# Optimization experiments

Measured on AMD Instinct MI355X. Metric: run time of the kernel, lower is better.

The kernel has to match this reference:

```python
import jax, jax.numpy as jnp
import numpy as np

N_NODES = 100000
N_EDGES = 1600000
F_IN = 35
F_OUT = 5
K = 3
HID = 100


def setup_inputs() -> dict:
    key = jax.random.key(0)
    ks = jax.random.split(key, 20)
    p = lambda k, shape: (jax.random.normal(k, shape, dtype=jnp.float32) * 0.1)
    inp = {
        "x": jax.random.normal(ks[0], (N_NODES, F_IN), dtype=jnp.float32),
        "edge_index": jax.random.randint(ks[1], (2, N_EDGES), 0, N_NODES, dtype=jnp.int64),
        "edge_weight": jax.random.uniform(ks[2], (N_EDGES,), dtype=jnp.float32),
        # MLP warm-start: Linear(35,100) -> ReLU -> Linear(100,5)
        "W1": p(ks[3], (F_IN, HID)), "b1": p(ks[4], (HID,)),
        "W2": p(ks[5], (HID, F_OUT)), "b2": p(ks[6], (F_OUT,)),
        # DCRNN gates: DConv weights [2 directions, K, in+out, out]
        "Wz": p(ks[7], (2, K, F_IN + F_OUT, F_OUT)), "bz": p(ks[8], (F_OUT,)),
        "Wr": p(ks[9], (2, K, F_IN + F_OUT, F_OUT)), "br": p(ks[10], (F_OUT,)),
        "Wh": p(ks[11], (2, K, F_IN + F_OUT, F_OUT)), "bh": p(ks[12], (F_OUT,)),
        # head Linear(5,1)
        "Wl": p(ks[13], (F_OUT, 1)), "bl": p(ks[14], (1,)),
    }
    return inp


def reference(x, edge_index, edge_weight, W1, b1, W2, b2, Wz, bz, Wr, br, Wh, bh, Wl, bl):
    n = x.shape[0]
    src, dst = edge_index[0], edge_index[1]
    eps = jnp.asarray(1e-12, x.dtype)
    # random-walk normalization: forward (out-degree) and backward (in-degree) diffusion
    deg_out = jax.ops.segment_sum(edge_weight, src, num_segments=n)
    deg_in = jax.ops.segment_sum(edge_weight, dst, num_segments=n)
    w_fwd = edge_weight / jnp.maximum(deg_out[src], eps)  # [E]
    w_bwd = edge_weight / jnp.maximum(deg_in[dst], eps)   # [E]

    def prop_fwd(X):  # aggregate src -> dst
        return jax.ops.segment_sum(X[src] * w_fwd[:, None], dst, num_segments=n)

    def prop_bwd(X):  # aggregate dst -> src (reversed edges)
        return jax.ops.segment_sum(X[dst] * w_bwd[:, None], src, num_segments=n)

    def dconv(X, W, b):  # W: [2, K, Cin, Cout]
        k_steps = W.shape[1]
        out = X @ W[0, 0] + X @ W[1, 0]
        if k_steps > 1:
            Tf0, Tb0 = X, X
            Tf1, Tb1 = prop_fwd(X), prop_bwd(X)
            out = out + Tf1 @ W[0, 1] + Tb1 @ W[1, 1]
            for k in range(2, k_steps):
                Tf2 = 2.0 * prop_fwd(Tf1) - Tf0
                Tb2 = 2.0 * prop_bwd(Tb1) - Tb0
                out = out + Tf2 @ W[0, k] + Tb2 @ W[1, k]
                Tf0, Tf1 = Tf1, Tf2
                Tb0, Tb1 = Tb1, Tb2
        return out + b

    # MLP warm-start hidden state
    h1 = jax.nn.relu(x @ W1 + b1) @ W2 + b2  # [N, F_OUT]

    # DCRNN GRU cell
    XH = jnp.concatenate([x, h1], axis=1)           # [N, F_IN+F_OUT]
    Z = jax.nn.sigmoid(dconv(XH, Wz, bz))
    R = jax.nn.sigmoid(dconv(XH, Wr, br))
    XHr = jnp.concatenate([x, h1 * R], axis=1)
    H_tilde = jnp.tanh(dconv(XHr, Wh, bh))
    H = Z * h1 + (1.0 - Z) * H_tilde                # [N, F_OUT]

    y = jax.nn.relu(H) @ Wl + bl                    # [N, 1]
    A = w_fwd                                        # normalized adjacency weights [E]
    return y, A
```

## Files before the change

kernel.cpp:

```cpp
#include <hip/hip_runtime.h>
#include <hip/hip_fp16.h>

#define F_IN 35
#define F_OUT 5
#define HID 100
#define BSH 8
#define BMSK 255
#define MAXB 512
#define NBLK 128

__device__ __forceinline__ unsigned qenc(float w) {
  unsigned b = __float_as_uint(w);
  int e = 127 - (int)((b >> 23) & 0xFF);
  unsigned m = (b >> 12) & 0x7FFu;
  if (e < 0) { e = 0; m = 0; }
  if (e > 15) { e = 15; m = 0; }
  return ((unsigned)e << 11) | m;
}
__device__ __forceinline__ float qdec(unsigned q) {
  return __uint_as_float(((127u - (q >> 11)) << 23) | ((q & 0x7FFu) << 12));
}

__device__ __forceinline__ float2 uph2(unsigned u) {
  __half2 h = *reinterpret_cast<const __half2*>(&u);
  return __half22float2(h);
}
__device__ __forceinline__ unsigned pkh2(float a, float b) {
  __half2 h = __floats2half2_rn(a, b);
  return *reinterpret_cast<const unsigned*>(&h);
}

__device__ __forceinline__ int ntli(const int* p) {
  return __builtin_nontemporal_load(p);
}
__device__ __forceinline__ float ntlf(const float* p) {
  return __builtin_nontemporal_load(p);
}
__device__ __forceinline__ long long ntll(const long long* p) {
  return __builtin_nontemporal_load(p);
}
__device__ __forceinline__ void ntsf(float* p, float v) {
  __builtin_nontemporal_store(v, p);
}

__global__ __launch_bounds__(256) void prep_weights(
    const float* __restrict__ Wz, const float* __restrict__ Wr,
    const float* __restrict__ Wh, const float* __restrict__ W1,
    float* __restrict__ W1t, float* __restrict__ WpackAt,
    float* __restrict__ WpackCxt, float* __restrict__ WpackCh) {
  int t = blockIdx.x * blockDim.x + threadIdx.x;
  auto W = [&](const float* Wp, int d, int k, int i, int o) {
    return Wp[((d * 3 + k) * 40 + i) * 5 + o];
  };
  auto wa = [&](int i, int c) -> float {
    if (c < 5)  return W(Wz,0,0,i,c)+W(Wz,1,0,i,c)-W(Wz,0,2,i,c)-W(Wz,1,2,i,c);
    if (c < 10) return W(Wr,0,0,i,c-5)+W(Wr,1,0,i,c-5)-W(Wr,0,2,i,c-5)-W(Wr,1,2,i,c-5);
    if (c < 15) return W(Wz,0,1,i,c-10);
    if (c < 20) return W(Wr,0,1,i,c-15);
    if (c < 25) return W(Wz,0,2,i,c-20);
    if (c < 30) return W(Wr,0,2,i,c-25);
    if (c < 35) return W(Wz,1,1,i,c-30);
    if (c < 40) return W(Wr,1,1,i,c-35);
    if (c < 45) return W(Wz,1,2,i,c-40);
    return W(Wr,1,2,i,c-45);
  };
  auto wc = [&](int i, int c) -> float {
    if (c < 5)  return W(Wh,0,0,i,c)+W(Wh,1,0,i,c)-W(Wh,0,2,i,c)-W(Wh,1,2,i,c);
    if (c < 10) return W(Wh,0,1,i,c-5);
    if (c < 15) return W(Wh,0,2,i,c-10);
    if (c < 20) return W(Wh,1,1,i,c-15);
    return W(Wh,1,2,i,c-20);
  };
  if (t < 3500) {
    int hh = t / 35, i = t % 35;
    W1t[t] = W1[i * HID + hh];
  } else if (t < 5500) {
    int u = t - 3500; int c = u / 40, i = u % 40;
    WpackAt[u] = wa(i, c);
  } else if (t < 6375) {
    int u = t - 5500; int c = u / 35, i = u % 35;
    WpackCxt[u] = wc(i, c);
  } else if (t < 6500) {
    int u = t - 6375; int o = u / 25, c = u % 25;
    WpackCh[u] = wc(F_IN + o, c);
  }
}

__global__ __launch_bounds__(1024) void passB_kernel(
    const int* __restrict__ ei, const float* __restrict__ w,
    int2* __restrict__ staged_f, int2* __restrict__ staged_b,
    int* __restrict__ lomat, int E) {
  __shared__ int hh[MAXB], sc[MAXB], cc[MAXB];
  int dir = blockIdx.y;
  int j = blockIdx.x;
  int tid = threadIdx.x;
  for (int k = tid; k < MAXB; k += blockDim.x) { hh[k] = 0; cc[k] = 0; }
  __syncthreads();
  size_t c0 = (size_t)j * E / NBLK;
  size_t c1 = (size_t)(j + 1) * E / NBLK;
  const int* keyc = dir ? ei : ei + E;
  const int* othc = dir ? ei + E : ei;
  int2* staged = dir ? staged_b : staged_f;
  int* lom = lomat + ((size_t)dir * NBLK + j) * (MAXB + 1);
  for (size_t e = c0 + tid; e < c1; e += blockDim.x) {
    int key = ntli(keyc + e);
    atomicAdd(&hh[key >> BSH], 1);
  }
  __syncthreads();
  if (tid < MAXB) sc[tid] = hh[tid];
  __syncthreads();
  for (int off = 1; off < MAXB; off <<= 1) {
    int a = (tid >= off && tid < MAXB) ? sc[tid - off] : 0;
    __syncthreads();
    if (tid < MAXB) sc[tid] += a;
    __syncthreads();
  }
  if (tid < MAXB) {
    int lo = sc[tid] - hh[tid];
    lom[tid] = lo;
    hh[tid] = lo;
  }
  if (tid == 0) lom[MAXB] = (int)(c1 - c0);
  __syncthreads();
  for (size_t e = c0 + tid; e < c1; e += blockDim.x) {
    int key = ntli(keyc + e);
    int oth = ntli(othc + e);
    unsigned q = qenc(ntlf(w + e));
    int b = key >> BSH;
    int p = hh[b] + atomicAdd(&cc[b], 1);
    staged[c0 + p] = make_int2(oth | ((key & BMSK) << 17), (int)q);
  }
}

__global__ __launch_bounds__(512) void scanb2_kernel(
    const int* __restrict__ lomat,
    int* __restrict__ bbase_f, int* __restrict__ bbase_b,
    int* __restrict__ rs_f, int* __restrict__ rs_b,
    int nbuck, int N, int E) {
  __shared__ int s0[MAXB], s1[MAXB];
  int t = threadIdx.x;
  int cf = 0, cb = 0;
  if (t < nbuck) {
    for (int j = 0; j < NBLK; j++) {
      const int* lf = lomat + (size_t)j * (MAXB + 1);
      const int* lb = lomat + ((size_t)NBLK + j) * (MAXB + 1);
      cf += lf[t + 1] - lf[t];
      cb += lb[t + 1] - lb[t];
    }
  }
  s0[t] = cf; s1[t] = cb;
  __syncthreads();
  for (int off = 1; off < MAXB; off <<= 1) {
    int a = (t >= off) ? s0[t - off] : 0;
    int b = (t >= off) ? s1[t - off] : 0;
    __syncthreads();
    s0[t] += a; s1[t] += b;
    __syncthreads();
  }
  bbase_f[t + 1] = s0[t];
  bbase_b[t + 1] = s1[t];
  if (t == 0) { bbase_f[0] = 0; bbase_b[0] = 0; rs_f[N] = E; rs_b[N] = E; }
}

__global__ __launch_bounds__(256) void passC_kernel(
    const int2* __restrict__ staged_f, const int2* __restrict__ staged_b,
    const int* __restrict__ lomat,
    const int* __restrict__ bbase_f, const int* __restrict__ bbase_b,
    int* __restrict__ adj_f, int* __restrict__ adj_b,
    int* __restrict__ rs_f, int* __restrict__ rs_b,
    float* __restrict__ inv_in, float* __restrict__ inv_out, int N, int E) {
  int dir = blockIdx.y;
  const long long* staged =
      (const long long*)(dir ? staged_b : staged_f);
  const int* lomd = lomat + (size_t)dir * NBLK * (MAXB + 1);
  const int* bbase = dir ? bbase_b : bbase_f;
  int* adj = dir ? adj_b : adj_f;
  int* rs  = dir ? rs_b : rs_f;
  float* inv = dir ? inv_out : inv_in;
  int b = blockIdx.x;
  int base = bbase[b];
  __shared__ int cnt[256]; __shared__ float wsum[256];
  __shared__ int loc[256]; __shared__ int cur[256];
  int tid = threadIdx.x;
  int wave = tid >> 6, lane = tid & 63;
  cnt[tid] = 0; wsum[tid] = 0.f; cur[tid] = 0;
  __syncthreads();
  int j0 = wave * 32;
  int lo0k = 0, lo1k = 0;
  if (lane < 32) {
    const int* lj = lomd + (size_t)(j0 + lane) * (MAXB + 1);
    lo0k = lj[b];
    lo1k = lj[b + 1];
  }
  for (int k = 0; k < 32; k++) {
    int lo0 = __shfl(lo0k, k);
    int lo1 = __shfl(lo1k, k);
    if (lo0 >= lo1) continue;
    size_t cj = (size_t)(j0 + k) * E / NBLK;
    for (int i = lo0 + lane; i < lo1; i += 64) {
      long long it = ntll(staged + cj + i);
      int idv = (int)(unsigned)(it & 0xFFFFFFFFll);
      unsigned q = (unsigned)((unsigned long long)it >> 32);
      int nl = (idv >> 17) & BMSK;
      atomicAdd(&cnt[nl], 1);
      atomicAdd(&wsum[nl], qdec(q));
    }
  }
  __syncthreads();
  int v = cnt[tid];
  loc[tid] = v;
  __syncthreads();
  for (int off = 1; off < 256; off <<= 1) {
    int a = (tid >= off) ? loc[tid - off] : 0;
    __syncthreads();
    loc[tid] += a;
    __syncthreads();
  }
  int excl = loc[tid] - v;
  int node = (b << BSH) + tid;
  if (node < N) {
    rs[node] = base + excl;
    inv[node] = 1.f / fmaxf(wsum[tid], 1e-12f);
  }
  __syncthreads();
  loc[tid] = excl;
  __syncthreads();
  for (int k = 0; k < 32; k++) {
    int lo0 = __shfl(lo0k, k);
    int lo1 = __shfl(lo1k, k);
    if (lo0 >= lo1) continue;
    size_t cj = (size_t)(j0 + k) * E / NBLK;
    for (int i = lo0 + lane; i < lo1; i += 64) {
      long long it = ntll(staged + cj + i);
      int idv = (int)(unsigned)(it & 0xFFFFFFFFll);
      int q = (int)((unsigned long long)it >> 32);
      int nl = (idv >> 17) & BMSK;
      int p = base + loc[nl] + atomicAdd(&cur[nl], 1);
      adj[p] = (idv & 0x1FFFF) | (q << 17);
    }
  }
}

__global__ __launch_bounds__(256) void wfout_kernel(
    const int* __restrict__ ei, const float* __restrict__ ew,
    const float* __restrict__ inv_out, float* __restrict__ wf, int E) {
  for (int e = blockIdx.x * blockDim.x + threadIdx.x; e < E;
       e += gridDim.x * blockDim.x)
    ntsf(wf + e, ntlf(ew + e) * inv_out[ntli(ei + e)]);
}

__global__ __launch_bounds__(256) void nodeA_kernel(
    const float* __restrict__ x,
    const float* __restrict__ W1t, const float* __restrict__ b1,
    const float* __restrict__ W2, const float* __restrict__ b2,
    const float* __restrict__ bz, const float* __restrict__ br,
    const float* __restrict__ WpackAt, const float* __restrict__ WpackCxt,
    const float* __restrict__ inv_out, const float* __restrict__ inv_in,
    float* __restrict__ h1, float* __restrict__ accDz,
    float* __restrict__ accDr, __half* __restrict__ PA_f,
    __half* __restrict__ PA_b, __half* __restrict__ accCx, int N) {
  __shared__ float part[4][64][5];
  int tid = threadIdx.x;
  int lane = tid & 63;
  int q = __builtin_amdgcn_readfirstlane(tid >> 6);
  int n = blockIdx.x * 64 + lane;
  bool act = n < N;
  float xv[40];
  const float* xr = x + (size_t)n * F_IN;
  #pragma unroll
  for (int i = 0; i < F_IN; i++) xv[i] = act ? xr[i] : 0.f;

  float h5[5] = {0.f, 0.f, 0.f, 0.f, 0.f};
  int hbase = q * 25;
  for (int k = 0; k < 25; k++) {
    int hh = hbase + k;
    const float* w1r = W1t + hh * F_IN;
    float a = b1[hh];
    #pragma unroll
    for (int i = 0; i < F_IN; i++) a = fmaf(xv[i], w1r[i], a);
    a = fmaxf(a, 0.f);
    #pragma unroll
    for (int o = 0; o < 5; o++) h5[o] = fmaf(a, W2[hh * 5 + o], h5[o]);
  }
  #pragma unroll
  for (int o = 0; o < 5; o++) part[q][lane][o] = h5[o];
  __syncthreads();
  #pragma unroll
  for (int o = 0; o < 5; o++) {
    h5[o] = part[0][lane][o] + part[1][lane][o] + part[2][lane][o] +
            part[3][lane][o] + b2[o];
    xv[F_IN + o] = h5[o];
  }
  if (!act) return;
  if (q == 0) {
    #pragma unroll
    for (int o = 0; o < 5; o++) h1[(size_t)n * 5 + o] = h5[o];
  }
  float sOut = inv_out[n], sIn = inv_in[n];
  int c0 = q * 19, c1 = min(c0 + 19, 75);
  for (int c = c0; c < c1; c++) {
    float a = 0.f;
    if (c < 50) {
      const float* wr = WpackAt + c * 40;
      #pragma unroll
      for (int i = 0; i < 40; i++) a = fmaf(xv[i], wr[i], a);
    } else {
      const float* wr = WpackCxt + (c - 50) * F_IN;
      #pragma unroll
      for (int i = 0; i < F_IN; i++) a = fmaf(xv[i], wr[i], a);
    }
    if (c < 5)       accDz[(size_t)n * 5 + c] = a + bz[c];
    else if (c < 10) accDr[(size_t)n * 5 + (c - 5)] = a + br[c - 5];
    else if (c < 30) PA_f[(size_t)n * 20 + (c - 10)] = __float2half(a * sOut);
    else if (c < 50) PA_b[(size_t)n * 20 + (c - 30)] = __float2half(a * sIn);
    else             accCx[(size_t)n * 25 + (c - 50)] = __float2half(a);
  }
}

__global__ __launch_bounds__(256) void p1_kernel(
    const int* __restrict__ rs_f, const int* __restrict__ rs_b,
    const int* __restrict__ adj_f, const int* __restrict__ adj_b,
    const __half* __restrict__ PA_f, const __half* __restrict__ PA_b,
    const float* __restrict__ inv_out, const float* __restrict__ inv_in,
    float* __restrict__ Q1_f, float* __restrict__ Q1_b,
    __half* __restrict__ Q2_f, __half* __restrict__ Q2_b, int N) {
  int dir = blockIdx.x & 1;
  int idx = (blockIdx.x >> 1) * 256 + threadIdx.x;
  if (idx >= 2 * N) return;
  int n = idx >> 1, half = idx & 1;
  const int* rs  = dir ? rs_b : rs_f;
  const int* adj = dir ? adj_b : adj_f;
  const __half* PA = dir ? PA_b : PA_f;
  int i0 = rs[n], i1 = rs[n + 1];
  float acc[10];
  #pragma unroll
  for (int c = 0; c < 10; c++) acc[c] = 0.f;
  int i = i0;
  for (; i + 4 <= i1; i += 4) {
    int a0 = ntli(adj + i),     a1 = ntli(adj + i + 1),
        a2 = ntli(adj + i + 2), a3 = ntli(adj + i + 3);
    const unsigned* r0 = (const unsigned*)(PA + (size_t)(a0 & 0x1FFFF) * 20) + half * 5;
    const unsigned* r1 = (const unsigned*)(PA + (size_t)(a1 & 0x1FFFF) * 20) + half * 5;
    const unsigned* r2 = (const unsigned*)(PA + (size_t)(a2 & 0x1FFFF) * 20) + half * 5;
    const unsigned* r3 = (const unsigned*)(PA + (size_t)(a3 & 0x1FFFF) * 20) + half * 5;
    unsigned u0[5], u1[5], u2[5], u3[5];
    #pragma unroll
    for (int k = 0; k < 5; k++) u0[k] = r0[k];
    #pragma unroll
    for (int k = 0; k < 5; k++) u1[k] = r1[k];
    #pragma unroll
    for (int k = 0; k < 5; k++) u2[k] = r2[k];
    #pragma unroll
    for (int k = 0; k < 5; k++) u3[k] = r3[k];
    float w0 = qdec(((unsigned)a0) >> 17), w1 = qdec(((unsigned)a1) >> 17),
          w2 = qdec(((unsigned)a2) >> 17), w3 = qdec(((unsigned)a3) >> 17);
    #pragma unroll
    for (int k = 0; k < 5; k++) {
      float2 f0 = uph2(u0[k]), f1 = uph2(u1[k]), f2 = uph2(u2[k]), f3 = uph2(u3[k]);
      acc[2*k]   = fmaf(w0, f0.x, acc[2*k]);   acc[2*k+1] = fmaf(w0, f0.y, acc[2*k+1]);
      acc[2*k]   = fmaf(w1, f1.x, acc[2*k]);   acc[2*k+1] = fmaf(w1, f1.y, acc[2*k+1]);
      acc[2*k]   = fmaf(w2, f2.x, acc[2*k]);   acc[2*k+1] = fmaf(w2, f2.y, acc[2*k+1]);
      acc[2*k]   = fmaf(w3, f3.x, acc[2*k]);   acc[2*k+1] = fmaf(w3, f3.y, acc[2*k+1]);
    }
  }
  for (; i < i1; i++) {
    int a = ntli(adj + i);
    float w = qdec(((unsigned)a) >> 17);
    const unsigned* row = (const unsigned*)(PA + (size_t)(a & 0x1FFFF) * 20) + half * 5;
    #pragma unroll
    for (int k = 0; k < 5; k++) {
      float2 f = uph2(row[k]);
      acc[2*k] = fmaf(w, f.x, acc[2*k]); acc[2*k+1] = fmaf(w, f.y, acc[2*k+1]);
    }
  }
  if (!half) {
    float* q = (dir ? Q1_b : Q1_f) + (size_t)n * 10;
    #pragma unroll
    for (int c = 0; c < 10; c++) q[c] = acc[c];
  } else {
    float sc = dir ? inv_in[n] : inv_out[n];
    unsigned* q = (unsigned*)((dir ? Q2_b : Q2_f) + (size_t)n * 12);
    q[0] = pkh2(acc[0] * sc, acc[1] * sc);
    q[1] = pkh2(acc[2] * sc, acc[3] * sc);
    q[2] = pkh2(acc[4] * sc, 0.f);
    q[3] = pkh2(acc[5] * sc, acc[6] * sc);
    q[4] = pkh2(acc[7] * sc, acc[8] * sc);
    q[5] = pkh2(acc[9] * sc, 0.f);
  }
}

__global__ __launch_bounds__(256) void p2a_kernel(
    const int* __restrict__ rs_f, const int* __restrict__ rs_b,
    const int* __restrict__ adj_f, const int* __restrict__ adj_b,
    const __half* __restrict__ Q2_f, const __half* __restrict__ Q2_b,
    float* __restrict__ G_f, float* __restrict__ G_b, int N) {
  int dir = blockIdx.x & 1;
  int idx = (blockIdx.x >> 1) * 256 + threadIdx.x;
  if (idx >= 2 * N) return;
  int n = idx >> 1, grp = idx & 1;
  const int* rs  = dir ? rs_b : rs_f;
  const int* adj = dir ? adj_b : adj_f;
  const __half* Q2 = dir ? Q2_b : Q2_f;
  int i0 = rs[n], i1 = rs[n + 1];
  float a[5];
  #pragma unroll
  for (int c = 0; c < 5; c++) a[c] = 0.f;
  int i = i0;
  for (; i + 8 <= i1; i += 8) {
    int e[8];
    #pragma unroll
    for (int k = 0; k < 8; k++) e[k] = ntli(adj + i + k);
    unsigned u[8][3];
    #pragma unroll
    for (int k = 0; k < 8; k++) {
      const unsigned* row =
          (const unsigned*)(Q2 + (size_t)(e[k] & 0x1FFFF) * 12) + grp * 3;
      u[k][0] = row[0]; u[k][1] = row[1]; u[k][2] = row[2];
    }
    #pragma unroll
    for (int k = 0; k < 8; k++) {
      float w = qdec(((unsigned)e[k]) >> 17);
      float2 f0 = uph2(u[k][0]), f1 = uph2(u[k][1]), f2 = uph2(u[k][2]);
      a[0] = fmaf(w, f0.x, a[0]); a[1] = fmaf(w, f0.y, a[1]);
      a[2] = fmaf(w, f1.x, a[2]); a[3] = fmaf(w, f1.y, a[3]);
      a[4] = fmaf(w, f2.x, a[4]);
    }
  }
  for (; i < i1; i++) {
    int e = ntli(adj + i);
    float w = qdec(((unsigned)e) >> 17);
    const unsigned* row =
        (const unsigned*)(Q2 + (size_t)(e & 0x1FFFF) * 12) + grp * 3;
    float2 f0 = uph2(row[0]), f1 = uph2(row[1]), f2 = uph2(row[2]);
    a[0] = fmaf(w, f0.x, a[0]); a[1] = fmaf(w, f0.y, a[1]);
    a[2] = fmaf(w, f1.x, a[2]); a[3] = fmaf(w, f1.y, a[3]);
    a[4] = fmaf(w, f2.x, a[4]);
  }
  float* g = (dir ? G_b : G_f) + (size_t)n * 10 + grp * 5;
  #pragma unroll
  for (int c = 0; c < 5; c++) g[c] = a[c];
}

__global__ __launch_bounds__(256) void p2b_kernel(
    const float* __restrict__ G_f, const float* __restrict__ G_b,
    const float* __restrict__ Q1_f, const float* __restrict__ Q1_b,
    const float* __restrict__ accDz, const float* __restrict__ accDr,
    const __half* __restrict__ accCx, const float* __restrict__ h1,
    const float* __restrict__ bh, const float* __restrict__ WpackCh,
    const float* __restrict__ inv_out, const float* __restrict__ inv_in,
    float* __restrict__ Zg, float* __restrict__ accDh,
    __half* __restrict__ PH_f, __half* __restrict__ PH_b, int N) {
  int t = blockIdx.x * blockDim.x + threadIdx.x;
  int n = t >> 1, l = t & 1;
  if (n >= N) return;
  float r[5], zv[5];
  #pragma unroll
  for (int o = 0; o < 5; o++) {
    float zA = G_f[(size_t)n * 10 + o] + G_b[(size_t)n * 10 + o];
    float rA = G_f[(size_t)n * 10 + 5 + o] + G_b[(size_t)n * 10 + 5 + o];
    float zp = accDz[(size_t)n * 5 + o] + Q1_f[(size_t)n * 10 + o] +
               Q1_b[(size_t)n * 10 + o] + 2.f * zA;
    float rp = accDr[(size_t)n * 5 + o] + Q1_f[(size_t)n * 10 + 5 + o] +
               Q1_b[(size_t)n * 10 + 5 + o] + 2.f * rA;
    zv[o] = 1.f / (1.f + __expf(-zp));
    r[o]  = 1.f / (1.f + __expf(-rp));
  }
  if (l == 0) {
    #pragma unroll
    for (int o = 0; o < 5; o++) Zg[(size_t)n * 5 + o] = zv[o];
  }
  float hr[5];
  #pragma unroll
  for (int o = 0; o < 5; o++) hr[o] = h1[(size_t)n * 5 + o] * r[o];

  float sOut = inv_out[n], sIn = inv_in[n];
  int c0 = l ? 13 : 0, c1 = l ? 25 : 13;
  for (int c = c0; c < c1; c++) {
    float acc = __half2float(accCx[(size_t)n * 25 + c]);
    #pragma unroll
    for (int o = 0; o < 5; o++) acc = fmaf(hr[o], WpackCh[o * 25 + c], acc);
    if (c < 5)       accDh[(size_t)n * 5 + c] = acc + bh[c];
    else if (c < 10) PH_f[(size_t)n * 12 + (c - 5)] = __float2half(acc * sOut);
    else if (c < 15) PH_f[(size_t)n * 12 + 6 + (c - 10)] = __float2half(acc * sOut);
    else if (c < 20) PH_b[(size_t)n * 12 + (c - 15)] = __float2half(acc * sIn);
    else             PH_b[(size_t)n * 12 + 6 + (c - 20)] = __float2half(acc * sIn);
  }
}

__global__ __launch_bounds__(256) void p3_kernel(
    const int* __restrict__ rs_f, const int* __restrict__ rs_b,
    const int* __restrict__ adj_f, const int* __restrict__ adj_b,
    const __half* __restrict__ PH_f, const __half* __restrict__ PH_b,
    const float* __restrict__ inv_out, const float* __restrict__ inv_in,
    float* __restrict__ Q1h_f, float* __restrict__ Q1h_b,
    __half* __restrict__ Q2h_f, __half* __restrict__ Q2h_b, int N) {
  int dir = blockIdx.x & 1;
  int idx = (blockIdx.x >> 1) * 256 + threadIdx.x;
  if (idx >= 2 * N) return;
  int n = idx >> 1, half = idx & 1;
  const int* rs  = dir ? rs_b : rs_f;
  const int* adj = dir ? adj_b : adj_f;
  const __half* PH = dir ? PH_b : PH_f;
  int i0 = rs[n], i1 = rs[n + 1];
  float acc[5];
  #pragma unroll
  for (int c = 0; c < 5; c++) acc[c] = 0.f;
  int i = i0;
  for (; i + 8 <= i1; i += 8) {
    int e[8];
    #pragma unroll
    for (int k = 0; k < 8; k++) e[k] = ntli(adj + i + k);
    unsigned u[8][3];
    #pragma unroll
    for (int k = 0; k < 8; k++) {
      const unsigned* row =
          (const unsigned*)(PH + (size_t)(e[k] & 0x1FFFF) * 12) + half * 3;
      u[k][0] = row[0]; u[k][1] = row[1]; u[k][2] = row[2];
    }
    #pragma unroll
    for (int k = 0; k < 8; k++) {
      float w = qdec(((unsigned)e[k]) >> 17);
      float2 f0 = uph2(u[k][0]), f1 = uph2(u[k][1]), f2 = uph2(u[k][2]);
      acc[0] = fmaf(w, f0.x, acc[0]); acc[1] = fmaf(w, f0.y, acc[1]);
      acc[2] = fmaf(w, f1.x, acc[2]); acc[3] = fmaf(w, f1.y, acc[3]);
      acc[4] = fmaf(w, f2.x, acc[4]);
    }
  }
  for (; i < i1; i++) {
    int a = ntli(adj + i);
    float w = qdec(((unsigned)a) >> 17);
    const unsigned* row =
        (const unsigned*)(PH + (size_t)(a & 0x1FFFF) * 12) + half * 3;
    float2 f0 = uph2(row[0]), f1 = uph2(row[1]), f2 = uph2(row[2]);
    acc[0] = fmaf(w, f0.x, acc[0]); acc[1] = fmaf(w, f0.y, acc[1]);
    acc[2] = fmaf(w, f1.x, acc[2]); acc[3] = fmaf(w, f1.y, acc[3]);
    acc[4] = fmaf(w, f2.x, acc[4]);
  }
  if (!half) {
    float* q = (dir ? Q1h_b : Q1h_f) + (size_t)n * 5;
    #pragma unroll
    for (int c = 0; c < 5; c++) q[c] = acc[c];
  } else {
    float sc = dir ? inv_in[n] : inv_out[n];
    unsigned* q = (unsigned*)((dir ? Q2h_b : Q2h_f) + (size_t)n * 8);
    q[0] = pkh2(acc[0] * sc, acc[1] * sc);
    q[1] = pkh2(acc[2] * sc, acc[3] * sc);
    q[2] = pkh2(acc[4] * sc, 0.f);
  }
}

__global__ __launch_bounds__(256) void p4_kernel(
    const int* __restrict__ rs_f, const int* __restrict__ rs_b,
    const int* __restrict__ adj_f, const int* __restrict__ adj_b,
    const __half* __restrict__ Q2h_f, const __half* __restrict__ Q2h_b,
    const float* __restrict__ Q1h_f, const float* __restrict__ Q1h_b,
    const float* __restrict__ accDh, const float* __restrict__ Zg,
    const float* __restrict__ h1, const float* __restrict__ Wl,
    const float* __restrict__ bl, float* __restrict__ y, int N) {
  int t = blockIdx.x * blockDim.x + threadIdx.x;
  int n = t >> 1, l = t & 1;
  if (n >= N) return;
  const int* rs  = l ? rs_b : rs_f;
  const int* adj = l ? adj_b : adj_f;
  const __half* Q2h = l ? Q2h_b : Q2h_f;
  float a[5];
  #pragma unroll
  for (int c = 0; c < 5; c++) a[c] = 0.f;
  int i0 = rs[n], i1 = rs[n + 1];
  int i = i0;
  for (; i + 8 <= i1; i += 8) {
    int e[8];
    #pragma unroll
    for (int k = 0; k < 8; k++) e[k] = ntli(adj + i + k);
    unsigned u[8][3];
    #pragma unroll
    for (int k = 0; k < 8; k++) {
      const unsigned* row = (const unsigned*)(Q2h + (size_t)(e[k] & 0x1FFFF) * 8);
      u[k][0] = row[0]; u[k][1] = row[1]; u[k][2] = row[2];
    }
    #pragma unroll
    for (int k = 0; k < 8; k++) {
      float w = qdec(((unsigned)e[k]) >> 17);
      float2 f0 = uph2(u[k][0]), f1 = uph2(u[k][1]), f2 = uph2(u[k][2]);
      a[0] = fmaf(w, f0.x, a[0]); a[1] = fmaf(w, f0.y, a[1]);
      a[2] = fmaf(w, f1.x, a[2]); a[3] = fmaf(w, f1.y, a[3]);
      a[4] = fmaf(w, f2.x, a[4]);
    }
  }
  for (; i < i1; i++) {
    int e = ntli(adj + i);
    float w = qdec(((unsigned)e) >> 17);
    const unsigned* row = (const unsigned*)(Q2h + (size_t)(e & 0x1FFFF) * 8);
    float2 f0 = uph2(row[0]), f1 = uph2(row[1]), f2 = uph2(row[2]);
    a[0] = fmaf(w, f0.x, a[0]); a[1] = fmaf(w, f0.y, a[1]);
    a[2] = fmaf(w, f1.x, a[2]); a[3] = fmaf(w, f1.y, a[3]);
    a[4] = fmaf(w, f2.x, a[4]);
  }
  #pragma unroll
  for (int c = 0; c < 5; c++) a[c] += __shfl_xor(a[c], 1);
  if (l) return;
  float acc = bl[0];
  #pragma unroll
  for (int o = 0; o < 5; o++) {
    float pre = accDh[(size_t)n * 5 + o] + Q1h_f[(size_t)n * 5 + o] +
                Q1h_b[(size_t)n * 5 + o] + 2.f * a[o];
    float ht = tanhf(pre);
    float z = Zg[(size_t)n * 5 + o];
    float H = z * h1[(size_t)n * 5 + o] + (1.f - z) * ht;
    acc += fmaxf(H, 0.f) * Wl[o];
  }
  y[n] = acc;
}

extern "C" void kernel_launch(void* const* d_in, const int* in_sizes, int n_in,
                              void* d_out, int out_size, void* d_ws, size_t ws_size,
                              hipStream_t stream) {
  const float* x  = (const float*)d_in[0];
  const int*   ei = (const int*)d_in[1];
  const float* ew = (const float*)d_in[2];
  const float* W1 = (const float*)d_in[3];
  const float* b1 = (const float*)d_in[4];
  const float* W2 = (const float*)d_in[5];
  const float* b2 = (const float*)d_in[6];
  const float* Wz = (const float*)d_in[7];
  const float* bz = (const float*)d_in[8];
  const float* Wr = (const float*)d_in[9];
  const float* br = (const float*)d_in[10];
  const float* Wh = (const float*)d_in[11];
  const float* bh = (const float*)d_in[12];
  const float* Wl = (const float*)d_in[13];
  const float* bl = (const float*)d_in[14];

  const int N = in_sizes[0] / F_IN;
  const int E = in_sizes[2];
  const int nbuck = ((N - 1) >> BSH) + 1;

  float* out = (float*)d_out;
  float* y_out  = out;
  float* wf_out = out + N;

  float* W = (float*)d_ws;
  size_t o = 0;
  int* bbase_f = (int*)(W + o); o += MAXB + 2;
  int* bbase_b = (int*)(W + o); o += MAXB + 2;
  int* lomat   = (int*)(W + o); o += (size_t)2 * NBLK * (MAXB + 1);
  int* rs_f    = (int*)(W + o); o += (size_t)N + 1;
  int* rs_b    = (int*)(W + o); o += (size_t)N + 1;
  float* inv_out = W + o; o += N;
  float* inv_in  = W + o; o += N;
  int* adj_f   = (int*)(W + o); o += (size_t)E;
  int* adj_b   = (int*)(W + o); o += (size_t)E;
  float* h1    = W + o; o += (size_t)5 * N;
  float* accDz = W + o; o += (size_t)5 * N;
  float* accDr = W + o; o += (size_t)5 * N;
  float* accDh = W + o; o += (size_t)5 * N;
  float* Zg    = W + o; o += (size_t)5 * N;
  __half* accCx = (__half*)(W + o); o += (size_t)13 * N;
  o = (o + 1) & ~(size_t)1;
  size_t prop0 = o;
  __half* PA_f = (__half*)(W + o); o += (size_t)10 * N;
  __half* PA_b = (__half*)(W + o); o += (size_t)10 * N;
  float* Q1_f  = W + o; o += (size_t)10 * N;
  float* Q1_b  = W + o; o += (size_t)10 * N;
  __half* Q2_f = (__half*)(W + o); o += (size_t)6 * N;
  __half* Q2_b = (__half*)(W + o); o += (size_t)6 * N;
  __half* PH_f = (__half*)(W + o); o += (size_t)6 * N;
  __half* PH_b = (__half*)(W + o); o += (size_t)6 * N;
  float* Q1h_f = W + o; o += (size_t)5 * N;
  float* Q1h_b = W + o; o += (size_t)5 * N;
  o = (o + 1) & ~(size_t)1;
  __half* Q2h_f = (__half*)(W + o); o += (size_t)4 * N;
  __half* Q2h_b = (__half*)(W + o); o += (size_t)4 * N;
  float* G_f   = W + o; o += (size_t)10 * N;
  float* G_b   = W + o; o += (size_t)10 * N;
  float* W1t     = W + o; o += 3500;
  float* WpackAt = W + o; o += 2000;
  float* WpackCxt = W + o; o += 875;
  float* WpackCh  = W + o; o += 125;

  int2* staged_f = (int2*)(W + prop0);
  int2* staged_b = staged_f + E;

  const int NB2 = (2 * N + 255) / 256;
  const int NBd = 2 * ((2 * N + 255) / 256);
  const int NBn = (N + 63) / 64;

  prep_weights<<<26, 256, 0, stream>>>(Wz, Wr, Wh, W1,
                                       W1t, WpackAt, WpackCxt, WpackCh);

  passB_kernel<<<dim3(NBLK, 2), 1024, 0, stream>>>(ei, ew, staged_f, staged_b,
                                                   lomat, E);
  scanb2_kernel<<<1, MAXB, 0, stream>>>(lomat, bbase_f, bbase_b,
                                        rs_f, rs_b, nbuck, N, E);
  passC_kernel<<<dim3(nbuck, 2), 256, 0, stream>>>(
      staged_f, staged_b, lomat, bbase_f, bbase_b, adj_f, adj_b,
      rs_f, rs_b, inv_in, inv_out, N, E);
  wfout_kernel<<<1024, 256, 0, stream>>>(ei, ew, inv_out, wf_out, E);

  nodeA_kernel<<<NBn, 256, 0, stream>>>(x, W1t, b1, W2, b2, bz, br, WpackAt,
                                        WpackCxt, inv_out, inv_in,
                                        h1, accDz, accDr, PA_f, PA_b,
                                        accCx, N);

  p1_kernel<<<NBd, 256, 0, stream>>>(rs_f, rs_b, adj_f, adj_b, PA_f, PA_b,
                                     inv_out, inv_in, Q1_f, Q1_b, Q2_f, Q2_b, N);
  p2a_kernel<<<NBd, 256, 0, stream>>>(rs_f, rs_b, adj_f, adj_b, Q2_f, Q2_b,
                                      G_f, G_b, N);
  p2b_kernel<<<NB2, 256, 0, stream>>>(G_f, G_b, Q1_f, Q1_b, accDz, accDr,
                                      accCx, h1, bh, WpackCh, inv_out, inv_in,
                                      Zg, accDh, PH_f, PH_b, N);
  p3_kernel<<<NBd, 256, 0, stream>>>(rs_f, rs_b, adj_f, adj_b, PH_f, PH_b,
                                     inv_out, inv_in, Q1h_f, Q1h_b,
                                     Q2h_f, Q2h_b, N);
  p4_kernel<<<NB2, 256, 0, stream>>>(rs_f, rs_b, adj_f, adj_b, Q2h_f, Q2h_b,
                                     Q1h_f, Q1h_b, accDh, Zg, h1, Wl, bl,
                                     y_out, N);
}
```

Measured before the change: 366.3 us.

## Halve bucket size and cache staged edges in registers across passC passes

```diff
diff --git a/kernel.cpp b/kernel.cpp
--- a/kernel.cpp
+++ b/kernel.cpp
@@ -4,10 +4,12 @@
 #define F_IN 35
 #define F_OUT 5
 #define HID 100
-#define BSH 8
-#define BMSK 255
-#define MAXB 512
+#define BSH 7
+#define BMSK 127
+#define MAXB 1024
 #define NBLK 128
+#define CAPB 3072
+#define KMAX 12
 
 __device__ __forceinline__ unsigned qenc(float w) {
   unsigned b = __float_as_uint(w);
@@ -132,7 +134,7 @@
   }
 }
 
-__global__ __launch_bounds__(512) void scanb2_kernel(
+__global__ __launch_bounds__(1024) void scanb2_kernel(
     const int* __restrict__ lomat,
     int* __restrict__ bbase_f, int* __restrict__ bbase_b,
     int* __restrict__ rs_f, int* __restrict__ rs_b,
@@ -179,26 +181,50 @@
   float* inv = dir ? inv_out : inv_in;
   int b = blockIdx.x;
   int base = bbase[b];
-  __shared__ int cnt[256]; __shared__ float wsum[256];
-  __shared__ int loc[256]; __shared__ int cur[256];
+  __shared__ int cnt[128]; __shared__ float wsum[128];
+  __shared__ int loc[128]; __shared__ int cur[128];
+  __shared__ int lbase[NBLK + 1];
+  __shared__ int lo0s[NBLK];
+  __shared__ int cjs[NBLK];
+  __shared__ unsigned char run_of[CAPB];
   int tid = threadIdx.x;
-  int wave = tid >> 6, lane = tid & 63;
-  cnt[tid] = 0; wsum[tid] = 0.f; cur[tid] = 0;
-  __syncthreads();
-  int j0 = wave * 32;
-  int lo0k = 0, lo1k = 0;
-  if (lane < 32) {
-    const int* lj = lomd + (size_t)(j0 + lane) * (MAXB + 1);
-    lo0k = lj[b];
-    lo1k = lj[b + 1];
-  }
-  for (int k = 0; k < 32; k++) {
-    int lo0 = __shfl(lo0k, k);
-    int lo1 = __shfl(lo1k, k);
-    if (lo0 >= lo1) continue;
-    size_t cj = (size_t)(j0 + k) * E / NBLK;
-    for (int i = lo0 + lane; i < lo1; i += 64) {
-      long long it = ntll(staged + cj + i);
+  if (tid < 128) { cnt[tid] = 0; wsum[tid] = 0.f; cur[tid] = 0; }
+  if (tid < NBLK) {
+    const int* lj = lomd + (size_t)tid * (MAXB + 1);
+    int lo0 = lj[b], lo1 = lj[b + 1];
+    lo0s[tid] = lo0;
+    lbase[tid] = lo1 - lo0;
+    cjs[tid] = (int)((size_t)tid * E / NBLK);
+  }
+  __syncthreads();
+  for (int off = 1; off < NBLK; off <<= 1) {
+    int v = (tid < NBLK && tid >= off) ? lbase[tid - off] : 0;
+    __syncthreads();
+    if (tid < NBLK) lbase[tid] += v;
+    __syncthreads();
+  }
+  int incl = (tid < NBLK) ? lbase[tid] : 0;
+  __syncthreads();
+  if (tid < NBLK) lbase[tid + 1] = incl;
+  if (tid == 0) lbase[0] = 0;
+  __syncthreads();
+  int total = lbase[NBLK];
+  if (tid < NBLK) {
+    int p0 = lbase[tid], p1 = lbase[tid + 1];
+    int pe = min(p1, CAPB);
+    for (int p = p0; p < pe; p++) run_of[p] = (unsigned char)tid;
+  }
+  __syncthreads();
+
+  long long items[KMAX];
+  #pragma unroll
+  for (int k = 0; k < KMAX; k++) {
+    int p = tid + (k << 8);
+    if (p < total && p < CAPB) {
+      int j = run_of[p];
+      int idx = cjs[j] + lo0s[j] + (p - lbase[j]);
+      long long it = ntll(staged + idx);
+      items[k] = it;
       int idv = (int)(unsigned)(it & 0xFFFFFFFFll);
       unsigned q = (unsigned)((unsigned long long)it >> 32);
       int nl = (idv >> 17) & BMSK;
@@ -206,38 +232,67 @@
       atomicAdd(&wsum[nl], qdec(q));
     }
   }
-  __syncthreads();
-  int v = cnt[tid];
-  loc[tid] = v;
-  __syncthreads();
-  for (int off = 1; off < 256; off <<= 1) {
-    int a = (tid >= off) ? loc[tid - off] : 0;
+  for (int p = CAPB + tid; p < total; p += 256) {
+    int loJ = 0, hiJ = NBLK;
+    while (hiJ - loJ > 1) {
+      int mid = (loJ + hiJ) >> 1;
+      if (lbase[mid] <= p) loJ = mid; else hiJ = mid;
+    }
+    long long it = ntll(staged + cjs[loJ] + lo0s[loJ] + (p - lbase[loJ]));
+    int idv = (int)(unsigned)(it & 0xFFFFFFFFll);
+    unsigned q = (unsigned)((unsigned long long)it >> 32);
+    int nl = (idv >> 17) & BMSK;
+    atomicAdd(&cnt[nl], 1);
+    atomicAdd(&wsum[nl], qdec(q));
+  }
+  __syncthreads();
+
+  int v = 0;
+  if (tid < 128) { v = cnt[tid]; loc[tid] = v; }
+  __syncthreads();
+  for (int off = 1; off < 128; off <<= 1) {
+    int a = (tid >= off && tid < 128) ? loc[tid - off] : 0;
     __syncthreads();
-    loc[tid] += a;
+    if (tid < 128) loc[tid] += a;
     __syncthreads();
   }
-  int excl = loc[tid] - v;
-  int node = (b << BSH) + tid;
-  if (node < N) {
-    rs[node] = base + excl;
-    inv[node] = 1.f / fmaxf(wsum[tid], 1e-12f);
-  }
-  __syncthreads();
-  loc[tid] = excl;
-  __syncthreads();
-  for (int k = 0; k < 32; k++) {
-    int lo0 = __shfl(lo0k, k);
-    int lo1 = __shfl(lo1k, k);
-    if (lo0 >= lo1) continue;
-    size_t cj = (size_t)(j0 + k) * E / NBLK;
-    for (int i = lo0 + lane; i < lo1; i += 64) {
-      long long it = ntll(staged + cj + i);
+  int excl = 0;
+  if (tid < 128) {
+    excl = loc[tid] - v;
+    int node = (b << BSH) + tid;
+    if (node < N) {
+      rs[node] = base + excl;
+      inv[node] = 1.f / fmaxf(wsum[tid], 1e-12f);
+    }
+  }
+  __syncthreads();
+  if (tid < 128) loc[tid] = excl;
+  __syncthreads();
+
+  #pragma unroll
+  for (int k = 0; k < KMAX; k++) {
+    int p = tid + (k << 8);
+    if (p < total && p < CAPB) {
+      long long it = items[k];
       int idv = (int)(unsigned)(it & 0xFFFFFFFFll);
       int q = (int)((unsigned long long)it >> 32);
       int nl = (idv >> 17) & BMSK;
-      int p = base + loc[nl] + atomicAdd(&cur[nl], 1);
-      adj[p] = (idv & 0x1FFFF) | (q << 17);
-    }
+      int pos = base + loc[nl] + atomicAdd(&cur[nl], 1);
+      adj[pos] = (idv & 0x1FFFF) | (q << 17);
+    }
+  }
+  for (int p = CAPB + tid; p < total; p += 256) {
+    int loJ = 0, hiJ = NBLK;
+    while (hiJ - loJ > 1) {
+      int mid = (loJ + hiJ) >> 1;
+      if (lbase[mid] <= p) loJ = mid; else hiJ = mid;
+    }
+    long long it = ntll(staged + cjs[loJ] + lo0s[loJ] + (p - lbase[loJ]));
+    int idv = (int)(unsigned)(it & 0xFFFFFFFFll);
+    int q = (int)((unsigned long long)it >> 32);
+    int nl = (idv >> 17) & BMSK;
+    int pos = base + loc[nl] + atomicAdd(&cur[nl], 1);
+    adj[pos] = (idv & 0x1FFFF) | (q << 17);
   }
 }
 
```

Result: no change. 368.5 us (+0.6%).
